# Kernel tuning notes

Measured on AMD Instinct MI355X. Metric: run time of the kernel, lower is better.

## Reference

```python
import jax, jax.numpy as jnp
import numpy as np

N = 100000
E = 3200000
IN, HID, OUT = 512, 256, 64
K = 10
ALPHA = 0.1


def setup_inputs() -> dict:
    key = jax.random.key(0)
    ks = jax.random.split(key, 8)
    x = jax.random.normal(ks[0], (N, IN), dtype=jnp.float32)
    edge_index = jax.random.randint(ks[1], (2, E), 0, N, dtype=jnp.int64)
    W1 = jax.random.normal(ks[2], (IN, HID), dtype=jnp.float32) / np.sqrt(IN)
    b1 = jnp.zeros((HID,), dtype=jnp.float32)
    W2 = jax.random.normal(ks[3], (HID, OUT), dtype=jnp.float32) / np.sqrt(HID)
    b2 = jnp.zeros((OUT,), dtype=jnp.float32)
    # PPR init: temp[k] = alpha*(1-alpha)^k, temp[K] = (1-alpha)^K
    temp = ALPHA * (1.0 - ALPHA) ** np.arange(K + 1)
    temp[-1] = (1.0 - ALPHA) ** K
    temp = jnp.asarray(temp, dtype=jnp.float32)
    return {"x": x, "edge_index": edge_index, "W1": W1, "b1": b1,
            "W2": W2, "b2": b2, "temp": temp}


def reference(x, edge_index, W1, b1, W2, b2, temp):
    n = x.shape[0]
    # MLP (dropout = identity in eval mode)
    h = jax.nn.relu(x @ W1 + b1) @ W2 + b2  # [N, OUT]

    # gcn_norm: add self-loops, edge_weight = 1, sym-normalize
    loops = jnp.arange(n, dtype=edge_index.dtype)
    row = jnp.concatenate([edge_index[0], loops])  # source (x_j)
    col = jnp.concatenate([edge_index[1], loops])  # target (aggregate into)
    w = jnp.ones(row.shape[0], dtype=h.dtype)
    deg = jax.ops.segment_sum(w, col, num_segments=n)
    dinv = jnp.where(deg > 0, jax.lax.rsqrt(deg), 0.0)
    norm = dinv[row] * w * dinv[col]  # [E+N]

    hidden = h * temp[0]

    def step(carry, gamma):
        cur, hid = carry
        msg = norm[:, None] * cur[row]                       # gather+scale
        cur = jax.ops.segment_sum(msg, col, num_segments=n)  # scatter-add
        hid = hid + gamma * cur
        return (cur, hid), None

    (_, hidden), _ = jax.lax.scan(step, (h, hidden), temp[1:])
    return hidden
```

## Files before the change

kernel.cpp:

```cpp
#include <hip/hip_runtime.h>
#include <hip/hip_bf16.h>

#define NN   100000
#define EE   3200000
#define INF  512
#define HIDF 256
#define OUTF 64
#define KSTEPS 10

typedef __attribute__((ext_vector_type(8))) short short8;
typedef __attribute__((ext_vector_type(4))) float floatx4;
typedef unsigned short ushort_t;

static __device__ inline short bf2s(__hip_bfloat16 h) {
    return __builtin_bit_cast(short, h);
}

static __device__ inline unsigned short f2bf(float f) {
    unsigned u = __float_as_uint(f);
    unsigned r = (u + 0x7FFFu + ((u >> 16) & 1u)) >> 16;
    return (unsigned short)r;
}

static __device__ inline float b2f(unsigned short u) {
    return __uint_as_float(((unsigned)u) << 16);
}


__global__ void zero_kernel(int* p, int n) {
    int i = blockIdx.x * 256 + threadIdx.x;
    if (i < n) p[i] = 0;
}

__global__ void count_kernel(const int* __restrict__ ei, int* __restrict__ counts) {
    int e = blockIdx.x * 256 + threadIdx.x;
    if (e < EE) atomicAdd(&counts[ei[EE + e]], 1);
}

__global__ void dinv_kernel(const int* __restrict__ counts, float* __restrict__ dinv) {
    int i = blockIdx.x * 256 + threadIdx.x;
    if (i < NN) dinv[i] = rsqrtf((float)(counts[i] + 1));
}

__global__ void scan1(const int* __restrict__ counts, int* __restrict__ offs,
                      int* __restrict__ partial) {
    __shared__ int s[256];
    int tid = threadIdx.x;
    int i = blockIdx.x * 256 + tid;
    int v = (i < NN) ? counts[i] : 0;
    s[tid] = v;
    __syncthreads();
    for (int d = 1; d < 256; d <<= 1) {
        int t = (tid >= d) ? s[tid - d] : 0;
        __syncthreads();
        s[tid] += t;
        __syncthreads();
    }
    if (i < NN) offs[i] = s[tid] - v;
    if (tid == 255) partial[blockIdx.x] = s[255];
}

__global__ void scan2(int* partial, int nblocks) {
    __shared__ int s[512];
    int tid = threadIdx.x;
    int v = (tid < nblocks) ? partial[tid] : 0;
    s[tid] = v;
    __syncthreads();
    for (int d = 1; d < 512; d <<= 1) {
        int t = (tid >= d) ? s[tid - d] : 0;
        __syncthreads();
        s[tid] += t;
        __syncthreads();
    }
    if (tid < nblocks) partial[tid] = s[tid] - v;
}

__global__ void scan3(int* __restrict__ offs, const int* __restrict__ partial) {
    int i = blockIdx.x * 256 + threadIdx.x;
    if (i < NN) offs[i] += partial[i >> 8];
    else if (i == NN) offs[NN] = EE;
}

__global__ void fill_kernel(const int* __restrict__ ei, const int* __restrict__ offs,
                            int* __restrict__ counts, int* __restrict__ srcIdx) {
    int e = blockIdx.x * 256 + threadIdx.x;
    if (e >= EE) return;
    int r = ei[e];
    int c = ei[EE + e];
    int old = atomicSub(&counts[c], 1);
    srcIdx[offs[c] + old - 1] = r;
}

__global__ void pack_w1(const float* __restrict__ W1, short* __restrict__ W1p) {
    int id = blockIdx.x * 256 + threadIdx.x;
    if (id >= INF * HIDF) return;
    int jj = id & 7, l = (id >> 3) & 15, q = (id >> 7) & 3, t = (id >> 9) & 15, kk = id >> 13;
    int k = kk * 32 + q * 8 + jj, n = t * 16 + l;
    W1p[id] = (short)f2bf(W1[k * HIDF + n]);
}

__global__ void pack_w2(const float* __restrict__ W2, short* __restrict__ W2p) {
    int id = blockIdx.x * 256 + threadIdx.x;
    if (id >= HIDF * OUTF) return;
    int jj = id & 7, l = (id >> 3) & 15, q = (id >> 7) & 3, t = (id >> 9) & 3, kk = id >> 11;
    int k = kk * 32 + q * 8 + jj, n = t * 16 + l;
    W2p[id] = (short)f2bf(W2[k * OUTF + n]);
}


__global__ __launch_bounds__(256) void mlp_kernel(
    const float* __restrict__ x, const short* __restrict__ W1p,
    const short* __restrict__ W2p, const float* __restrict__ b1,
    const float* __restrict__ b2, const float* __restrict__ temp,
    const float* __restrict__ dinv,
    ushort_t* __restrict__ z0, float* __restrict__ out) {

    __shared__ __align__(16) short hlds[64][HIDF + 8];

    int tid = threadIdx.x;
    int wave = tid >> 6, lane = tid & 63;
    int l16 = lane & 15, quad = lane >> 4;
    int brow = blockIdx.x * 64;

    const floatx4 zf = {0.f, 0.f, 0.f, 0.f};
    floatx4 acc[4][4];
#pragma unroll
    for (int mi = 0; mi < 4; mi++)
#pragma unroll
        for (int j = 0; j < 4; j++) acc[mi][j] = zf;

    const float* rp[4];
#pragma unroll
    for (int mi = 0; mi < 4; mi++) {
        int row = brow + mi * 16 + l16;
        if (row > NN - 1) row = NN - 1;
        rp[mi] = x + (size_t)row * INF + quad * 8;
    }

    for (int kk = 0; kk < 16; kk++) {
        short8 a[4];
#pragma unroll
        for (int mi = 0; mi < 4; mi++) {
            const float4* ap = reinterpret_cast<const float4*>(rp[mi] + kk * 32);
            float4 f0 = ap[0];
            float4 f1 = ap[1];
            __hip_bfloat162 q0 = __float22bfloat162_rn(make_float2(f0.x, f0.y));
            __hip_bfloat162 q1 = __float22bfloat162_rn(make_float2(f0.z, f0.w));
            __hip_bfloat162 q2 = __float22bfloat162_rn(make_float2(f1.x, f1.y));
            __hip_bfloat162 q3 = __float22bfloat162_rn(make_float2(f1.z, f1.w));
            short8 av;
            av[0] = bf2s(q0.x); av[1] = bf2s(q0.y);
            av[2] = bf2s(q1.x); av[3] = bf2s(q1.y);
            av[4] = bf2s(q2.x); av[5] = bf2s(q2.y);
            av[6] = bf2s(q3.x); av[7] = bf2s(q3.y);
            a[mi] = av;
        }
        short8 b[4];
#pragma unroll
        for (int j = 0; j < 4; j++) {
            int t = wave * 4 + j;
            b[j] = *reinterpret_cast<const short8*>(
                W1p + (((size_t)(kk * 16 + t) * 64 + quad * 16 + l16) << 3));
        }
#pragma unroll
        for (int mi = 0; mi < 4; mi++)
#pragma unroll
            for (int j = 0; j < 4; j++)
                acc[mi][j] = __builtin_amdgcn_mfma_f32_16x16x32_bf16(a[mi], b[j], acc[mi][j], 0, 0, 0);
    }

#pragma unroll
    for (int j = 0; j < 4; j++) {
        float bj = b1[wave * 64 + j * 16 + l16];
#pragma unroll
        for (int mi = 0; mi < 4; mi++)
#pragma unroll
            for (int r = 0; r < 4; r++) {
                float v = acc[mi][j][r] + bj;
                v = fmaxf(v, 0.f);
                hlds[mi * 16 + quad * 4 + r][wave * 64 + j * 16 + l16] = (short)f2bf(v);
            }
    }
    __syncthreads();

    floatx4 acc2[4];
#pragma unroll
    for (int j = 0; j < 4; j++) acc2[j] = zf;

#pragma unroll
    for (int kk = 0; kk < 8; kk++) {
        short8 a2 = *reinterpret_cast<const short8*>(&hlds[wave * 16 + l16][kk * 32 + quad * 8]);
#pragma unroll
        for (int j = 0; j < 4; j++) {
            short8 bb = *reinterpret_cast<const short8*>(
                W2p + (((size_t)(kk * 4 + j) * 64 + quad * 16 + l16) << 3));
            acc2[j] = __builtin_amdgcn_mfma_f32_16x16x32_bf16(a2, bb, acc2[j], 0, 0, 0);
        }
    }

    float t0 = temp[0];
#pragma unroll
    for (int j = 0; j < 4; j++) {
        float bb = b2[j * 16 + l16];
#pragma unroll
        for (int r = 0; r < 4; r++) {
            int row = brow + wave * 16 + quad * 4 + r;
            if (row < NN) {
                float v = acc2[j][r] + bb;
                size_t o = (size_t)row * 64 + j * 16 + l16;
                out[o] = t0 * v;
                z0[o] = f2bf(dinv[row] * v);
            }
        }
    }
}


__global__ __launch_bounds__(256) void prop_kernel(
    const int* __restrict__ srcIdx, const int* __restrict__ offs,
    const float* __restrict__ dinv, const ushort_t* __restrict__ z,
    ushort_t* __restrict__ zn, float* __restrict__ hid,
    const float* __restrict__ temp, int k, int write_z) {

    int node = blockIdx.x * 4 + (threadIdx.x >> 6);
    if (node >= NN) return;
    int f = threadIdx.x & 63;
    int beg = __builtin_amdgcn_readfirstlane(offs[node]);
    int end = __builtin_amdgcn_readfirstlane(offs[node + 1]);
    size_t o = (size_t)node * 64 + f;
    float acc = b2f(z[o]);

    int e = beg;
    for (; e + 4 <= end; e += 4) {
        int s0 = srcIdx[e];
        int s1 = srcIdx[e + 1];
        int s2 = srcIdx[e + 2];
        int s3 = srcIdx[e + 3];
        float v0 = b2f(z[(size_t)s0 * 64 + f]);
        float v1 = b2f(z[(size_t)s1 * 64 + f]);
        float v2 = b2f(z[(size_t)s2 * 64 + f]);
        float v3 = b2f(z[(size_t)s3 * 64 + f]);
        acc += v0 + v1 + v2 + v3;
    }
    for (; e < end; ++e) {
        acc += b2f(z[(size_t)srcIdx[e] * 64 + f]);
    }

    float dv = dinv[node];
    float cn = dv * acc;
    hid[o] += temp[k] * cn;
    if (write_z) zn[o] = f2bf(dv * cn);
}


extern "C" void kernel_launch(void* const* d_in, const int* in_sizes, int n_in,
                              void* d_out, int out_size, void* d_ws, size_t ws_size,
                              hipStream_t stream) {
    const float* x    = (const float*)d_in[0];
    const int*   ei   = (const int*)d_in[1];
    const float* W1   = (const float*)d_in[2];
    const float* b1   = (const float*)d_in[3];
    const float* W2   = (const float*)d_in[4];
    const float* b2   = (const float*)d_in[5];
    const float* temp = (const float*)d_in[6];
    float* out = (float*)d_out;

    char* p = (char*)d_ws;
    auto carve = [&](size_t bytes) -> char* {
        char* r = p;
        p += (bytes + 255) & ~(size_t)255;
        return r;
    };
    ushort_t* zA   = (ushort_t*)carve(sizeof(ushort_t) * (size_t)NN * 64);
    ushort_t* zB   = (ushort_t*)carve(sizeof(ushort_t) * (size_t)NN * 64);
    int* srcIdx    = (int*)carve(sizeof(int) * (size_t)EE);
    int* counts    = (int*)carve(sizeof(int) * NN);
    int* offs      = (int*)carve(sizeof(int) * (NN + 1));
    int* partial   = (int*)carve(sizeof(int) * 512);
    float* dinv    = (float*)carve(sizeof(float) * NN);
    short* W1p     = (short*)carve(sizeof(short) * INF * HIDF);
    short* W2p     = (short*)carve(sizeof(short) * HIDF * OUTF);

    const int NB = (NN + 255) / 256;

    zero_kernel<<<NB, 256, 0, stream>>>(counts, NN);
    pack_w1<<<(INF * HIDF + 255) / 256, 256, 0, stream>>>(W1, W1p);
    pack_w2<<<(HIDF * OUTF + 255) / 256, 256, 0, stream>>>(W2, W2p);

    count_kernel<<<EE / 256, 256, 0, stream>>>(ei, counts);
    dinv_kernel<<<NB, 256, 0, stream>>>(counts, dinv);
    scan1<<<NB, 256, 0, stream>>>(counts, offs, partial);
    scan2<<<1, 512, 0, stream>>>(partial, NB);
    scan3<<<(NN + 256) / 256, 256, 0, stream>>>(offs, partial);
    fill_kernel<<<EE / 256, 256, 0, stream>>>(ei, offs, counts, srcIdx);

    mlp_kernel<<<(NN + 63) / 64, 256, 0, stream>>>(x, W1p, W2p, b1, b2, temp, dinv, zA, out);

    ushort_t* a = zA;
    ushort_t* b = zB;
    for (int k = 1; k <= KSTEPS; k++) {
        prop_kernel<<<NN / 4, 256, 0, stream>>>(srcIdx, offs, dinv, a, b, out, temp, k,
                                                (k < KSTEPS) ? 1 : 0);
        ushort_t* t = a; a = b; b = t;
    }
}
```

Baseline: 1.431 ms.

## Gather 8 neighbors per wave with 16-byte row loads and shuffle-reduce

New measurement: 1.295 ms. 1.1x faster.

```diff
diff --git a/kernel.cpp b/kernel.cpp
--- a/kernel.cpp
+++ b/kernel.cpp
@@ -216,40 +216,93 @@
 }
 
 
-__global__ __launch_bounds__(256) void prop_kernel(
+#define BLO(u) __uint_as_float((u) << 16)
+#define BHI(u) __uint_as_float((u) & 0xFFFF0000u)
+#define ACC8(v)                      \
+    do {                             \
+        a0 += BLO((v).x);            \
+        a1 += BHI((v).x);            \
+        a2 += BLO((v).y);            \
+        a3 += BHI((v).y);            \
+        a4 += BLO((v).z);            \
+        a5 += BHI((v).z);            \
+        a6 += BLO((v).w);            \
+        a7 += BHI((v).w);            \
+    } while (0)
+
+__global__ __launch_bounds__(256, 8) void prop_kernel(
     const int* __restrict__ srcIdx, const int* __restrict__ offs,
     const float* __restrict__ dinv, const ushort_t* __restrict__ z,
     ushort_t* __restrict__ zn, float* __restrict__ hid,
     const float* __restrict__ temp, int k, int write_z) {
 
     int node = blockIdx.x * 4 + (threadIdx.x >> 6);
-    if (node >= NN) return;
-    int f = threadIdx.x & 63;
+    int lane = threadIdx.x & 63;
+    int g = lane >> 3;
+    int q = lane & 7;
+
     int beg = __builtin_amdgcn_readfirstlane(offs[node]);
     int end = __builtin_amdgcn_readfirstlane(offs[node + 1]);
-    size_t o = (size_t)node * 64 + f;
-    float acc = b2f(z[o]);
+
+    float a0 = 0.f, a1 = 0.f, a2 = 0.f, a3 = 0.f;
+    float a4 = 0.f, a5 = 0.f, a6 = 0.f, a7 = 0.f;
+
+    {
+        uint4 v = reinterpret_cast<const uint4*>(z + ((size_t)node << 6))[q];
+        if (g == 0) ACC8(v);
+    }
 
     int e = beg;
-    for (; e + 4 <= end; e += 4) {
-        int s0 = srcIdx[e];
-        int s1 = srcIdx[e + 1];
-        int s2 = srcIdx[e + 2];
-        int s3 = srcIdx[e + 3];
-        float v0 = b2f(z[(size_t)s0 * 64 + f]);
-        float v1 = b2f(z[(size_t)s1 * 64 + f]);
-        float v2 = b2f(z[(size_t)s2 * 64 + f]);
-        float v3 = b2f(z[(size_t)s3 * 64 + f]);
-        acc += v0 + v1 + v2 + v3;
-    }
-    for (; e < end; ++e) {
-        acc += b2f(z[(size_t)srcIdx[e] * 64 + f]);
+    for (; e + 16 <= end; e += 16) {
+        int s0 = srcIdx[e + g];
+        int s1 = srcIdx[e + 8 + g];
+        uint4 v0 = reinterpret_cast<const uint4*>(z + ((size_t)s0 << 6))[q];
+        uint4 v1 = reinterpret_cast<const uint4*>(z + ((size_t)s1 << 6))[q];
+        ACC8(v0);
+        ACC8(v1);
+    }
+    for (; e < end; e += 8) {
+        int ee = e + g;
+        int cl = (ee < end) ? ee : (end - 1);
+        int s = srcIdx[cl];
+        uint4 v = reinterpret_cast<const uint4*>(z + ((size_t)s << 6))[q];
+        if (ee < end) ACC8(v);
+    }
+
+#pragma unroll
+    for (int m = 8; m < 64; m <<= 1) {
+        a0 += __shfl_xor(a0, m);
+        a1 += __shfl_xor(a1, m);
+        a2 += __shfl_xor(a2, m);
+        a3 += __shfl_xor(a3, m);
+        a4 += __shfl_xor(a4, m);
+        a5 += __shfl_xor(a5, m);
+        a6 += __shfl_xor(a6, m);
+        a7 += __shfl_xor(a7, m);
     }
 
     float dv = dinv[node];
-    float cn = dv * acc;
-    hid[o] += temp[k] * cn;
-    if (write_z) zn[o] = f2bf(dv * cn);
+    float tk = temp[k];
+    float c0 = dv * a0, c1 = dv * a1, c2 = dv * a2, c3 = dv * a3;
+    float c4 = dv * a4, c5 = dv * a5, c6 = dv * a6, c7 = dv * a7;
+
+    if (g == 0) {
+        float* hp = hid + ((size_t)node << 6) + q * 8;
+        float4 h0 = *reinterpret_cast<float4*>(hp);
+        float4 h1 = *reinterpret_cast<float4*>(hp + 4);
+        h0.x += tk * c0; h0.y += tk * c1; h0.z += tk * c2; h0.w += tk * c3;
+        h1.x += tk * c4; h1.y += tk * c5; h1.z += tk * c6; h1.w += tk * c7;
+        *reinterpret_cast<float4*>(hp) = h0;
+        *reinterpret_cast<float4*>(hp + 4) = h1;
+        if (write_z) {
+            uint4 u;
+            u.x = (unsigned)f2bf(dv * c0) | ((unsigned)f2bf(dv * c1) << 16);
+            u.y = (unsigned)f2bf(dv * c2) | ((unsigned)f2bf(dv * c3) << 16);
+            u.z = (unsigned)f2bf(dv * c4) | ((unsigned)f2bf(dv * c5) << 16);
+            u.w = (unsigned)f2bf(dv * c6) | ((unsigned)f2bf(dv * c7) << 16);
+            reinterpret_cast<uint4*>(zn + ((size_t)node << 6))[q] = u;
+        }
+    }
 }
 
 
```
